# Kernel tuning notes

Hardware: AMD Instinct MI355X
Metric: run time of the kernel (lower is better)

## Reference

```python
import jax, jax.numpy as jnp
import numpy as np

# ---- static problem sizes (full batches: cum[b] = b * max_num) ----
B = 256          # graphs per batch
MAXN, MAXE, MAXC = 128, 256, 64   # max nodes / edges / 2-cells per graph
H = 256          # embed_dim == hidden
L = 4            # num GCNCConv layers
OUT = 10         # out_size
P_N, P_E = 131072, 98304          # up-adjacency pair counts (dim 0, dim 1)
Q_E, Q_C = 131072, 65536          # boundary incidence counts (dim 1, dim 2)


def setup_inputs() -> dict:
    key = jax.random.key(0)
    ks = jax.random.split(key, 24)
    s = 1.0 / np.sqrt(H)
    inp = {}
    # flat cochain features [total_entities, H]
    inp['x_n'] = jax.random.normal(ks[0], (B * MAXN, H), jnp.float32)
    inp['x_e'] = jax.random.normal(ks[1], (B * MAXE, H), jnp.float32)
    inp['x_c'] = jax.random.normal(ks[2], (B * MAXC, H), jnp.float32)
    # node-level up adjacency (pairs of nodes sharing an edge coboundary)
    inp['n_up_b'] = jax.random.randint(ks[3], (P_N,), 0, B, jnp.int32)
    inp['n_up_i'] = jax.random.randint(ks[4], (P_N,), 0, MAXN, jnp.int32)
    inp['n_up_j'] = jax.random.randint(ks[5], (P_N,), 0, MAXN, jnp.int32)
    inp['n_up_e'] = jax.random.randint(ks[6], (P_N,), 0, MAXE, jnp.int32)
    # edge-level up adjacency (pairs of edges sharing a cell coboundary)
    inp['e_up_b'] = jax.random.randint(ks[7], (P_E,), 0, B, jnp.int32)
    inp['e_up_i'] = jax.random.randint(ks[8], (P_E,), 0, MAXE, jnp.int32)
    inp['e_up_j'] = jax.random.randint(ks[9], (P_E,), 0, MAXE, jnp.int32)
    inp['e_up_c'] = jax.random.randint(ks[10], (P_E,), 0, MAXC, jnp.int32)
    # boundary incidence: edges -> nodes, cells -> edges
    inp['eb_b'] = jax.random.randint(ks[11], (Q_E,), 0, B, jnp.int32)
    inp['eb_i'] = jax.random.randint(ks[12], (Q_E,), 0, MAXE, jnp.int32)
    inp['eb_j'] = jax.random.randint(ks[13], (Q_E,), 0, MAXN, jnp.int32)
    inp['cb_b'] = jax.random.randint(ks[14], (Q_C,), 0, B, jnp.int32)
    inp['cb_i'] = jax.random.randint(ks[15], (Q_C,), 0, MAXC, jnp.int32)
    inp['cb_j'] = jax.random.randint(ks[16], (Q_C,), 0, MAXE, jnp.int32)
    # learned parameters
    inp['Wself'] = jax.random.normal(ks[17], (L, 3, H, H), jnp.float32) * s
    inp['bself'] = jnp.zeros((L, 3, H), jnp.float32)
    inp['Wupx'] = jax.random.normal(ks[18], (L, 2, H, H), jnp.float32) * s
    inp['Wupa'] = jax.random.normal(ks[19], (L, 2, H, H), jnp.float32) * s
    inp['Wb'] = jax.random.normal(ks[20], (L, 2, H, H), jnp.float32) * s
    inp['Wp'] = jax.random.normal(ks[21], (H, H), jnp.float32) * s
    inp['Wp_ref'] = jax.random.normal(ks[22], (H, H), jnp.float32) * s
    inp['bp'] = jnp.zeros((H,), jnp.float32)
    k2 = jax.random.split(ks[23], 4)
    inp['W1'] = jax.random.normal(k2[0], (3, H, 2 * H), jnp.float32) * s
    inp['b1'] = jnp.zeros((3, 2 * H), jnp.float32)
    inp['W2'] = jax.random.normal(k2[1], (2 * H, OUT), jnp.float32) * s
    inp['b2'] = jnp.zeros((OUT,), jnp.float32)
    return inp


def reference(x_n, x_e, x_c, n_up_b, n_up_i, n_up_j, n_up_e,
              e_up_b, e_up_i, e_up_j, e_up_c, eb_b, eb_i, eb_j,
              cb_b, cb_i, cb_j, Wself, bself, Wupx, Wupa, Wb,
              Wp, Wp_ref, bp, W1, b1, W2, b2):
    relu = jax.nn.relu
    # dense per-batch boundary adjacencies (scatter-set, as in init_data_to_dense_gcnc)
    b_adj_e = jnp.zeros((B, MAXE, MAXN), jnp.float32).at[eb_b, eb_i, eb_j].set(1.0)
    b_adj_c = jnp.zeros((B, MAXC, MAXE), jnp.float32).at[cb_b, cb_i, cb_j].set(1.0)
    # flat gather/scatter indices: cum[b] = b * max_num (full batches)
    n_i = n_up_b * MAXN + n_up_i
    n_j = n_up_b * MAXN + n_up_j
    n_a = n_up_b * MAXE + n_up_e   # up_attr_idx into edge features
    e_i = e_up_b * MAXE + e_up_i
    e_j = e_up_b * MAXE + e_up_j
    e_a = e_up_b * MAXC + e_up_c   # up_attr_idx into cell features
    xs = [x_n, x_e, x_c]
    refs = xs  # init features used by pool_weight
    for l in range(L):
        xn, xe, xc = xs
        # up messages: msg = relu(W x_j + W' up_attr), scatter-sum to receiver
        up_n = jax.ops.segment_sum(
            relu(xn[n_j] @ Wupx[l, 0] + xe[n_a] @ Wupa[l, 0]),
            n_i, num_segments=B * MAXN)
        up_e = jax.ops.segment_sum(
            relu(xe[e_j] @ Wupx[l, 1] + xc[e_a] @ Wupa[l, 1]),
            e_i, num_segments=B * MAXE)
        # boundary messages: dense masked matmul with incidence matrices
        bd_e = jnp.einsum('ben,bnh->beh', b_adj_e,
                          xn.reshape(B, MAXN, H)).reshape(B * MAXE, H) @ Wb[l, 0]
        bd_c = jnp.einsum('bce,beh->bch', b_adj_c,
                          xe.reshape(B, MAXE, H)).reshape(B * MAXC, H) @ Wb[l, 1]
        xs = [relu(xn @ Wself[l, 0] + bself[l, 0] + up_n),
              relu(xe @ Wself[l, 1] + bself[l, 1] + up_e + bd_e),
              relu(xc @ Wself[l, 2] + bself[l, 2] + bd_c)]
    # pool weights (gating vs. init features) + sum readout per dimension
    maxs = (MAXN, MAXE, MAXC)
    pooled = []
    for i in range(3):
        w = jax.nn.sigmoid(xs[i] @ Wp + refs[i] @ Wp_ref + bp)
        pooled.append((w * xs[i]).reshape(B, maxs[i], H).sum(axis=1))  # [B,H]
    h = sum(relu(pooled[i] @ W1[i] + b1[i]) for i in range(3))  # final_readout='sum'
    return h @ W2 + b2  # [B, OUT]
```

## Files before the change

kernel.cpp:

```cpp
#include <hip/hip_runtime.h>
#include <cstdint>
#include <cstddef>

typedef unsigned short u16;
typedef __bf16 bf16x8 __attribute__((ext_vector_type(8)));
typedef float f32x4 __attribute__((ext_vector_type(4)));
typedef unsigned short u16x8 __attribute__((ext_vector_type(8)));

#define NB   256
#define MAXN 128
#define MAXE 256
#define MAXC 64
#define HD   256
#define NLAYER 4
#define PN 131072
#define PE 98304
#define QE 131072
#define QC 65536
#define MN (NB*MAXN)
#define ME (NB*MAXE)
#define MC (NB*MAXC)

#define SEG_N  0
#define SEG_E  (MN)
#define SEG_EB (MN + ME)
#define SEG_CB (MN + 2*ME)
#define HTOT   (MN + 2*ME + MC)
#define UPTOT  (PN + PE)

__device__ __forceinline__ float bf2f(u16 u){
  union{unsigned int i; float f;} x; x.i = ((unsigned int)u) << 16; return x.f;
}
__device__ __forceinline__ u16 f2bf(float f){
  union{float f; unsigned int i;} x; x.f = f;
  unsigned int r = x.i + 0x7fffu + ((x.i >> 16) & 1u);
  return (u16)(r >> 16);
}
__device__ __forceinline__ f32x4 MFMA(bf16x8 a, bf16x8 b, f32x4 c){
  return __builtin_amdgcn_mfma_f32_16x16x32_bf16(a, b, c, 0, 0, 0);
}
__device__ __forceinline__ void gl_lds16(const u16* g, u16* l){
  __builtin_amdgcn_global_load_lds(
      (const __attribute__((address_space(1))) unsigned int*)g,
      (__attribute__((address_space(3))) unsigned int*)l, 16, 0, 0);
}

__global__ void detect_dtype(const u16* __restrict__ x, int* __restrict__ flag){
  if(threadIdx.x == 0 && blockIdx.x == 0){
    int cnt = 0;
    for(int i = 0; i < 64; i++){
      int e = (x[i] >> 7) & 0xFF;
      if(e >= 118 && e <= 136) cnt++;
    }
    *flag = (cnt >= 50) ? 1 : 0;
  }
}

__global__ __launch_bounds__(256) void conv_bf(const void* __restrict__ src, u16* __restrict__ dst,
                                               long n, const int* __restrict__ flag){
  long i = ((long)blockIdx.x * 256 + threadIdx.x) * 8;
  if(i >= n) return;
  const int isbf = *flag;
  if(i + 8 <= n){
    if(isbf){
      *reinterpret_cast<u16x8*>(dst + i) = *reinterpret_cast<const u16x8*>((const u16*)src + i);
    }else{
      const float* s = (const float*)src + i;
      float4 a = *reinterpret_cast<const float4*>(s);
      float4 b = *reinterpret_cast<const float4*>(s + 4);
      u16x8 o;
      o[0]=f2bf(a.x); o[1]=f2bf(a.y); o[2]=f2bf(a.z); o[3]=f2bf(a.w);
      o[4]=f2bf(b.x); o[5]=f2bf(b.y); o[6]=f2bf(b.z); o[7]=f2bf(b.w);
      *reinterpret_cast<u16x8*>(dst + i) = o;
    }
  }else{
    for(long e = i; e < n; e++)
      dst[e] = isbf ? ((const u16*)src)[e] : f2bf(((const float*)src)[e]);
  }
}

__global__ __launch_bounds__(256) void conv_f2b(const float* __restrict__ s, u16* __restrict__ d, long n){
  long i = ((long)blockIdx.x * 256 + threadIdx.x) * 8;
  if(i >= n) return;
  float4 a = *reinterpret_cast<const float4*>(s + i);
  float4 b = *reinterpret_cast<const float4*>(s + i + 4);
  u16x8 o;
  o[0]=f2bf(a.x); o[1]=f2bf(a.y); o[2]=f2bf(a.z); o[3]=f2bf(a.w);
  o[4]=f2bf(b.x); o[5]=f2bf(b.y); o[6]=f2bf(b.z); o[7]=f2bf(b.w);
  *reinterpret_cast<u16x8*>(d + i) = o;
}

__global__ __launch_bounds__(256) void zero_f4(float* __restrict__ p, long n4){
  long i = (long)blockIdx.x * blockDim.x + threadIdx.x;
  if(i >= n4) return;
  float4 z = {0.f, 0.f, 0.f, 0.f};
  *reinterpret_cast<float4*>(p + i * 4) = z;
}

__global__ void wt_transpose(const void* __restrict__ src, u16* __restrict__ dst,
                             const int* __restrict__ flag){
  __shared__ u16 t[16][17];
  int m = blockIdx.z;
  int n0 = blockIdx.x * 16, k0 = blockIdx.y * 16;
  size_t sidx = (size_t)m * 65536 + (size_t)(k0 + threadIdx.y) * 256 + n0 + threadIdx.x;
  u16 v = (*flag) ? ((const u16*)src)[sidx] : f2bf(((const float*)src)[sidx]);
  t[threadIdx.y][threadIdx.x] = v;
  __syncthreads();
  dst[(size_t)m * 65536 + (size_t)(n0 + threadIdx.y) * 256 + (k0 + threadIdx.x)] =
      t[threadIdx.x][threadIdx.y];
}

__global__ void w1_transpose(const u16* __restrict__ src, u16* __restrict__ dst){
  __shared__ u16 t[16][17];
  int i = blockIdx.z;
  int o0 = blockIdx.x * 16, k0 = blockIdx.y * 16;
  t[threadIdx.y][threadIdx.x] =
      src[(size_t)i * 131072 + (size_t)(k0 + threadIdx.y) * 512 + o0 + threadIdx.x];
  __syncthreads();
  dst[(size_t)i * 131072 + (size_t)(o0 + threadIdx.y) * 256 + (k0 + threadIdx.x)] =
      t[threadIdx.x][threadIdx.y];
}

__global__ void dedup_kernel(const int* __restrict__ bb, const int* __restrict__ bi,
                             const int* __restrict__ bj, unsigned int* __restrict__ mask,
                             unsigned char* __restrict__ valid, int Q, int maxI, int maxJ){
  int q = blockIdx.x * blockDim.x + threadIdx.x;
  if(q >= Q) return;
  int s = (bb[q] * maxI + bi[q]) * maxJ + bj[q];
  unsigned int bit = 1u << (s & 31);
  unsigned int old = atomicOr(&mask[s >> 5], bit);
  valid[q] = (old & bit) ? 0 : 1;
}

__global__ __launch_bounds__(256) void hist_up(const int* __restrict__ pb, const int* __restrict__ pi,
                                               int maxI, int segBase, int* __restrict__ hist, int P){
  int p = blockIdx.x * 256 + threadIdx.x;
  if(p >= P) return;
  atomicAdd(&hist[segBase + pb[p] * maxI + pi[p]], 1);
}
__global__ __launch_bounds__(256) void hist_bd(const int* __restrict__ bb, const int* __restrict__ bi,
                                               const unsigned char* __restrict__ valid,
                                               int maxI, int segBase, int* __restrict__ hist, int Q){
  int q = blockIdx.x * 256 + threadIdx.x;
  if(q >= Q || !valid[q]) return;
  atomicAdd(&hist[segBase + bb[q] * maxI + bi[q]], 1);
}

__global__ __launch_bounds__(256) void scan1(const int* __restrict__ hist, int* __restrict__ bsum){
  __shared__ int s[256];
  int t = threadIdx.x;
  long base = (long)blockIdx.x * 1024 + t * 4;
  int4 v = *reinterpret_cast<const int4*>(hist + base);
  s[t] = v.x + v.y + v.z + v.w;
  __syncthreads();
  for(int st = 128; st > 0; st >>= 1){
    if(t < st) s[t] += s[t + st];
    __syncthreads();
  }
  if(t == 0) bsum[blockIdx.x] = s[0];
}
__global__ __launch_bounds__(256) void scan2(int* __restrict__ bsum, int nb){
  __shared__ int s[256];
  int t = threadIdx.x;
  int v = (t < nb) ? bsum[t] : 0;
  s[t] = v;
  __syncthreads();
  for(int st = 1; st < 256; st <<= 1){
    int u = (t >= st) ? s[t - st] : 0;
    __syncthreads();
    s[t] += u;
    __syncthreads();
  }
  if(t < nb) bsum[t] = s[t] - v;
}
__global__ __launch_bounds__(256) void scan3(const int* __restrict__ hist, const int* __restrict__ bsum,
                                             int* __restrict__ off, int* __restrict__ cur){
  __shared__ int s[256];
  int t = threadIdx.x;
  long base = (long)blockIdx.x * 1024 + t * 4;
  int4 v = *reinterpret_cast<const int4*>(hist + base);
  int sum = v.x + v.y + v.z + v.w;
  s[t] = sum;
  __syncthreads();
  for(int st = 1; st < 256; st <<= 1){
    int u = (t >= st) ? s[t - st] : 0;
    __syncthreads();
    s[t] += u;
    __syncthreads();
  }
  int excl = s[t] - sum + bsum[blockIdx.x];
  int4 o;
  o.x = excl; o.y = o.x + v.x; o.z = o.y + v.y; o.w = o.z + v.z;
  *reinterpret_cast<int4*>(off + base) = o;
  *reinterpret_cast<int4*>(cur + base) = o;
}

__global__ __launch_bounds__(256) void fill_up(const int* __restrict__ pb, const int* __restrict__ pi,
    const int* __restrict__ pj, const int* __restrict__ pa, int maxI, int maxA, int segBase,
    int* __restrict__ cur, int2* __restrict__ csrUp, int P){
  int p = blockIdx.x * 256 + threadIdx.x;
  if(p >= P) return;
  int b = pb[p];
  int pos = atomicAdd(&cur[segBase + b * maxI + pi[p]], 1);
  int2 e; e.x = b * maxI + pj[p]; e.y = b * maxA + pa[p];
  csrUp[pos] = e;
}
__global__ __launch_bounds__(256) void fill_bd(const int* __restrict__ bb, const int* __restrict__ bi,
    const int* __restrict__ bj, const unsigned char* __restrict__ valid, int maxI, int maxJ,
    int segBase, int* __restrict__ cur, int* __restrict__ csrBd, int Q){
  int q = blockIdx.x * 256 + threadIdx.x;
  if(q >= Q || !valid[q]) return;
  int b = bb[q];
  int pos = atomicAdd(&cur[segBase + b * maxI + bi[q]], 1);
  csrBd[pos - UPTOT] = b * maxJ + bj[q];
}

template<int HAS_UP, int HAS_BD>
__global__ __launch_bounds__(256) void gather_k(
    const u16* __restrict__ Y, const u16* __restrict__ Z, const u16* __restrict__ BD,
    const int2* __restrict__ csrUp, const int* __restrict__ csrBd,
    const int* __restrict__ off, const int* __restrict__ deg,
    int upBase, int bdBase, u16* __restrict__ ACC, int rowLo){
  const int nb = gridDim.x;
  int bx = blockIdx.x;
  if((nb & 7) == 0) bx = (bx & 7) * (nb >> 3) + (bx >> 3);
  const int row = rowLo + bx * 4 + (threadIdx.x >> 6);
  const int lane = threadIdx.x & 63;
  const int c = lane * 4;
  float a0 = 0.f, a1 = 0.f, a2 = 0.f, a3 = 0.f;
  if(HAS_UP){
    int s = off[upBase + row];
    int d = deg[upBase + row];
    for(int k = 0; k < d; k++){
      int2 e = csrUp[s + k];
      const ushort4 y = *reinterpret_cast<const ushort4*>(Y + (size_t)e.x * 256 + c);
      const ushort4 z = *reinterpret_cast<const ushort4*>(Z + (size_t)e.y * 256 + c);
      a0 += fmaxf(bf2f(y.x) + bf2f(z.x), 0.f);
      a1 += fmaxf(bf2f(y.y) + bf2f(z.y), 0.f);
      a2 += fmaxf(bf2f(y.z) + bf2f(z.z), 0.f);
      a3 += fmaxf(bf2f(y.w) + bf2f(z.w), 0.f);
    }
  }
  if(HAS_BD){
    int s = off[bdBase + row] - UPTOT;
    int d = deg[bdBase + row];
    for(int k = 0; k < d; k++){
      int j = csrBd[s + k];
      const ushort4 x = *reinterpret_cast<const ushort4*>(BD + (size_t)j * 256 + c);
      a0 += bf2f(x.x); a1 += bf2f(x.y); a2 += bf2f(x.z); a3 += bf2f(x.w);
    }
  }
  ushort4 o; o.x = f2bf(a0); o.y = f2bf(a1); o.z = f2bf(a2); o.w = f2bf(a3);
  *reinterpret_cast<ushort4*>(ACC + (size_t)(row - rowLo) * 256 + c) = o;
}

template<int MODE>
__global__ __launch_bounds__(256) void gemm_b(const u16* A, const u16* __restrict__ WT,
                                              u16* C, const u16* __restrict__ ACC,
                                              const u16* __restrict__ bias,
                                              const u16* A2, const u16* __restrict__ WT2){
  __shared__ u16 lA[2][64 * 64];
  __shared__ u16 lB[2][256 * 64];
  const int t = threadIdx.x;
  const int lane = t & 63, wv = t >> 6;
  const int wn = wv;
  const int r = lane & 15, q = lane >> 4;
  const int rsw = r & 7;
  const size_t m0 = (size_t)blockIdx.x * 64;
  const int lrow = lane >> 3, lchk = lane & 7;
  const int csw = lchk ^ lrow;

  f32x4 acc[4][4];
#pragma unroll
  for(int i = 0; i < 4; i++)
#pragma unroll
    for(int j = 0; j < 4; j++) acc[i][j] = {0.f, 0.f, 0.f, 0.f};

  const int NT = (MODE == 3) ? 8 : 4;

  auto stage = [&](int tt, int buf){
    const u16* Ap = (MODE == 3 && tt >= 4) ? A2 : A;
    const u16* Wp = (MODE == 3 && tt >= 4) ? WT2 : WT;
    const int k0 = (tt & 3) * 64;
#pragma unroll
    for(int i = 0; i < 2; i++){
      const int row = wv * 16 + i * 8 + lrow;
      gl_lds16(Ap + (m0 + row) * 256 + k0 + csw * 8, &lA[buf][(wv * 16 + i * 8) * 64]);
    }
#pragma unroll
    for(int j = 0; j < 8; j++){
      const int n = wv * 64 + j * 8 + lrow;
      gl_lds16(Wp + (size_t)n * 256 + k0 + csw * 8, &lB[buf][(wv * 64 + j * 8) * 64]);
    }
  };

  stage(0, 0);
  stage(1, 1);

#pragma unroll
  for(int tt = 0; tt < NT; tt++){
    const int cur = tt & 1;
    if(tt < NT - 1) asm volatile("s_waitcnt vmcnt(10)" ::: "memory");
    else            asm volatile("s_waitcnt vmcnt(0)" ::: "memory");
    __builtin_amdgcn_s_barrier();
    __builtin_amdgcn_s_setprio(1);
#pragma unroll
    for(int ks = 0; ks < 2; ks++){
      bf16x8 af[4], bfr[4];
#pragma unroll
      for(int i = 0; i < 4; i++)
        af[i] = *reinterpret_cast<const bf16x8*>(
            &lA[cur][(i * 16 + r) * 64 + (((ks * 4 + q) ^ rsw) * 8)]);
#pragma unroll
      for(int j = 0; j < 4; j++)
        bfr[j] = *reinterpret_cast<const bf16x8*>(
            &lB[cur][(wn * 64 + j * 16 + r) * 64 + (((ks * 4 + q) ^ rsw) * 8)]);
#pragma unroll
      for(int i = 0; i < 4; i++)
#pragma unroll
        for(int j = 0; j < 4; j++) acc[i][j] = MFMA(bfr[j], af[i], acc[i][j]);
    }
    __builtin_amdgcn_s_setprio(0);
    __builtin_amdgcn_s_barrier();
    if(tt + 2 < NT) stage(tt + 2, cur);
  }

#pragma unroll
  for(int i = 0; i < 4; i++){
    const size_t row = m0 + i * 16 + r;
#pragma unroll
    for(int j = 0; j < 4; j++){
      const int col = wn * 64 + j * 16 + q * 4;
      const size_t idx = row * 256 + col;
      f32x4 v = acc[i][j];
      ushort4 o;
      if(MODE == 2){
        const ushort4 a4 = *reinterpret_cast<const ushort4*>(ACC + idx);
        const ushort4 b4 = *reinterpret_cast<const ushort4*>(bias + col);
        o.x = f2bf(fmaxf(v[0] + bf2f(a4.x) + bf2f(b4.x), 0.f));
        o.y = f2bf(fmaxf(v[1] + bf2f(a4.y) + bf2f(b4.y), 0.f));
        o.z = f2bf(fmaxf(v[2] + bf2f(a4.z) + bf2f(b4.z), 0.f));
        o.w = f2bf(fmaxf(v[3] + bf2f(a4.w) + bf2f(b4.w), 0.f));
      }else{
        o.x = f2bf(v[0]); o.y = f2bf(v[1]); o.z = f2bf(v[2]); o.w = f2bf(v[3]);
      }
      *reinterpret_cast<ushort4*>(C + idx) = o;
    }
  }
}

__global__ __launch_bounds__(256) void pool_reduce(const u16* __restrict__ G, const u16* __restrict__ bpv,
    const u16* __restrict__ X, float* __restrict__ pooled, int maxR, int rowsPerBlk){
  int b = blockIdx.x, h = threadIdx.x;
  int r0 = blockIdx.y * rowsPerBlk;
  float bias = bf2f(bpv[h]);
  float acc = 0.f;
  for(int r = r0; r < r0 + rowsPerBlk; r++){
    size_t o = ((size_t)b * maxR + r) * 256 + h;
    float t = bf2f(G[o]) + bias;
    float w = 1.f / (1.f + __expf(-t));
    acc += w * bf2f(X[o]);
  }
  atomicAdd(&pooled[b * 256 + h], acc);
}

__global__ __launch_bounds__(512) void readout1_mfma(const u16* __restrict__ Ab,
                                                     const u16* __restrict__ W1t,
                                                     const u16* __restrict__ b1,
                                                     float* __restrict__ hbuf){
  __shared__ u16 lA[2][128 * 64];
  __shared__ u16 lB[2][256 * 64];
  const int t = threadIdx.x;
  const int lane = t & 63, wv = t >> 6;
  const int wm = wv >> 2, wn = wv & 3;
  const int r = lane & 15, q = lane >> 4;
  const int rsw = r & 7;
  const int b0 = blockIdx.x * 128;
  const int o0 = blockIdx.y * 256;
  const int lrow = lane >> 3, lchk = lane & 7;
  const int csw = lchk ^ lrow;

  f32x4 acc[4][4], facc[4][4];
#pragma unroll
  for(int i = 0; i < 4; i++)
#pragma unroll
    for(int j = 0; j < 4; j++){ acc[i][j] = {0.f,0.f,0.f,0.f}; facc[i][j] = {0.f,0.f,0.f,0.f}; }

  auto stage = [&](int tt, int buf){
    const int ii = tt >> 2, k0 = (tt & 3) * 64;
    const u16* Ap = Ab + (size_t)ii * 65536;
    const u16* Wp = W1t + (size_t)ii * 131072;
#pragma unroll
    for(int i = 0; i < 2; i++){
      const int row = i * 64 + wv * 8 + lrow;
      gl_lds16(Ap + (size_t)(b0 + row) * 256 + k0 + csw * 8, &lA[buf][(i * 64 + wv * 8) * 64]);
    }
#pragma unroll
    for(int j = 0; j < 4; j++){
      const int n = j * 64 + wv * 8 + lrow;
      gl_lds16(Wp + (size_t)(o0 + n) * 256 + k0 + csw * 8, &lB[buf][(j * 64 + wv * 8) * 64]);
    }
  };

  stage(0, 0);
  stage(1, 1);

#pragma unroll
  for(int tt = 0; tt < 12; tt++){
    const int cur = tt & 1;
    if(tt < 11) asm volatile("s_waitcnt vmcnt(6)" ::: "memory");
    else        asm volatile("s_waitcnt vmcnt(0)" ::: "memory");
    __builtin_amdgcn_s_barrier();
#pragma unroll
    for(int ks = 0; ks < 2; ks++){
      bf16x8 af[4], bfr[4];
#pragma unroll
      for(int i = 0; i < 4; i++)
        af[i] = *reinterpret_cast<const bf16x8*>(
            &lA[cur][(wm * 64 + i * 16 + r) * 64 + (((ks * 4 + q) ^ rsw) * 8)]);
#pragma unroll
      for(int j = 0; j < 4; j++)
        bfr[j] = *reinterpret_cast<const bf16x8*>(
            &lB[cur][(wn * 64 + j * 16 + r) * 64 + (((ks * 4 + q) ^ rsw) * 8)]);
#pragma unroll
      for(int i = 0; i < 4; i++)
#pragma unroll
        for(int j = 0; j < 4; j++) acc[i][j] = MFMA(bfr[j], af[i], acc[i][j]);
    }
    if((tt & 3) == 3){
      const int ib = tt >> 2;
#pragma unroll
      for(int i = 0; i < 4; i++)
#pragma unroll
        for(int j = 0; j < 4; j++){
          const int col = o0 + wn * 64 + j * 16 + q * 4;
          const ushort4 b4 = *reinterpret_cast<const ushort4*>(b1 + ib * 512 + col);
          facc[i][j][0] += fmaxf(acc[i][j][0] + bf2f(b4.x), 0.f);
          facc[i][j][1] += fmaxf(acc[i][j][1] + bf2f(b4.y), 0.f);
          facc[i][j][2] += fmaxf(acc[i][j][2] + bf2f(b4.z), 0.f);
          facc[i][j][3] += fmaxf(acc[i][j][3] + bf2f(b4.w), 0.f);
          acc[i][j] = {0.f, 0.f, 0.f, 0.f};
        }
    }
    __builtin_amdgcn_s_barrier();
    if(tt + 2 < 12) stage(tt + 2, cur);
  }

#pragma unroll
  for(int i = 0; i < 4; i++){
    const int row = b0 + wm * 64 + i * 16 + r;
#pragma unroll
    for(int j = 0; j < 4; j++){
      const int col = o0 + wn * 64 + j * 16 + q * 4;
      *reinterpret_cast<f32x4*>(hbuf + (size_t)row * 512 + col) = facc[i][j];
    }
  }
}

__global__ __launch_bounds__(64) void readout2(const float* __restrict__ hbuf, const u16* __restrict__ W2,
                                               const u16* __restrict__ b2, void* __restrict__ out,
                                               const int* __restrict__ flag){
  int b = blockIdx.x, o = threadIdx.x;
  if(o >= 10) return;
  float a = bf2f(b2[o]);
  for(int k = 0; k < 512; k++) a += hbuf[(size_t)b * 512 + k] * bf2f(W2[k * 10 + o]);
  if(*flag) ((u16*)out)[b * 10 + o] = f2bf(a);
  else      ((float*)out)[b * 10 + o] = a;
}

extern "C" void kernel_launch(void* const* d_in, const int* in_sizes, int n_in,
                              void* d_out, int out_size, void* d_ws, size_t ws_size,
                              hipStream_t stream){
  const void* x_n = d_in[0];
  const void* x_e = d_in[1];
  const void* x_c = d_in[2];
  const int* n_up_b = (const int*)d_in[3];
  const int* n_up_i = (const int*)d_in[4];
  const int* n_up_j = (const int*)d_in[5];
  const int* n_up_e = (const int*)d_in[6];
  const int* e_up_b = (const int*)d_in[7];
  const int* e_up_i = (const int*)d_in[8];
  const int* e_up_j = (const int*)d_in[9];
  const int* e_up_c = (const int*)d_in[10];
  const int* eb_b = (const int*)d_in[11];
  const int* eb_i = (const int*)d_in[12];
  const int* eb_j = (const int*)d_in[13];
  const int* cb_b = (const int*)d_in[14];
  const int* cb_i = (const int*)d_in[15];
  const int* cb_j = (const int*)d_in[16];

  char* base = (char*)d_ws; size_t off0 = 0;
  auto alloc = [&](size_t n)->char*{ char* p = base + off0; off0 = (off0 + n + 255) & ~(size_t)255; return p; };
  u16* xn = (u16*)alloc((size_t)MN * HD * 2);
  u16* xe = (u16*)alloc((size_t)ME * HD * 2);
  u16* xc = (u16*)alloc((size_t)MC * HD * 2);
  u16* BIG1 = (u16*)alloc((size_t)ME * HD * 2);
  u16* SMa  = (u16*)alloc((size_t)MN * HD * 2);
  u16* SMb  = (u16*)alloc((size_t)MN * HD * 2);
  u16* ACC  = (u16*)alloc((size_t)16384 * HD * 4);
  u16* wt = (u16*)alloc((size_t)38 * 65536 * 2);
  unsigned int* mask_e = (unsigned int*)alloc((size_t)NB * MAXE * MAXN / 8);
  unsigned int* mask_c = (unsigned int*)alloc((size_t)NB * MAXC * MAXE / 8);
  unsigned char* valid_e = (unsigned char*)alloc(QE);
  unsigned char* valid_c = (unsigned char*)alloc(QC);
  float* pooled = (float*)alloc((size_t)3 * NB * HD * 4);
  float* hbuf   = (float*)alloc((size_t)NB * 512 * 4);
  int* flag     = (int*)alloc(256);
  int2* csrUp   = (int2*)alloc((size_t)UPTOT * 8);
  int* csrBd    = (int*)alloc((size_t)(QE + QC) * 4);
  int* hist     = (int*)alloc((size_t)HTOT * 4);
  int* offA     = (int*)alloc((size_t)HTOT * 4);
  int* bsum     = (int*)alloc(1024);
  u16* W1t      = (u16*)alloc((size_t)3 * 512 * 256 * 2);
  u16* pooledb  = (u16*)alloc((size_t)3 * NB * HD * 2);
  int* cur      = (int*)pooled;

  u16* wtSelf = wt;
  u16* wtUpx  = wt + (size_t)12 * 65536;
  u16* wtUpa  = wt + (size_t)20 * 65536;
  u16* wtB    = wt + (size_t)28 * 65536;
  u16* wtP    = wt + (size_t)36 * 65536;
  u16* wtPref = wt + (size_t)37 * 65536;

  u16* W1c = (u16*)mask_e;
  u16* b1c = W1c + 393216;
  u16* W2c = b1c + 1536;
  u16* b2c = W2c + 5120;
  u16* bsc = b2c + 16;
  u16* bpc = bsc + 3072;

  auto convN = [&](const void* s, u16* d, long n){
    long blk = (n + 8*256 - 1) / (8*256);
    conv_bf<<<(int)blk, 256, 0, stream>>>(s, d, n, flag);
  };

  detect_dtype<<<1, 64, 0, stream>>>((const u16*)x_n, flag);
  zero_f4<<<(65536 + 255)/256, 256, 0, stream>>>((float*)mask_e, 65536);
  zero_f4<<<(32768 + 255)/256, 256, 0, stream>>>((float*)mask_c, 32768);
  dedup_kernel<<<QE/256, 256, 0, stream>>>(eb_b, eb_i, eb_j, mask_e, valid_e, QE, MAXE, MAXN);
  dedup_kernel<<<QC/256, 256, 0, stream>>>(cb_b, cb_i, cb_j, mask_c, valid_c, QC, MAXC, MAXE);

  wt_transpose<<<dim3(16,16,12), dim3(16,16), 0, stream>>>(d_in[17], wtSelf, flag);
  wt_transpose<<<dim3(16,16,8),  dim3(16,16), 0, stream>>>(d_in[19], wtUpx,  flag);
  wt_transpose<<<dim3(16,16,8),  dim3(16,16), 0, stream>>>(d_in[20], wtUpa,  flag);
  wt_transpose<<<dim3(16,16,8),  dim3(16,16), 0, stream>>>(d_in[21], wtB,    flag);
  wt_transpose<<<dim3(16,16,1),  dim3(16,16), 0, stream>>>(d_in[22], wtP,    flag);
  wt_transpose<<<dim3(16,16,1),  dim3(16,16), 0, stream>>>(d_in[23], wtPref, flag);
  convN(x_n, xn, (long)MN * HD);
  convN(x_e, xe, (long)ME * HD);
  convN(x_c, xc, (long)MC * HD);
  convN(d_in[18], bsc, 3072);
  convN(d_in[24], bpc, 256);
  convN(d_in[25], W1c, 393216);
  convN(d_in[26], b1c, 1536);
  convN(d_in[27], W2c, 5120);
  convN(d_in[28], b2c, 10);
  w1_transpose<<<dim3(32,16,3), dim3(16,16), 0, stream>>>(W1c, W1t);

  zero_f4<<<(HTOT/4 + 255)/256, 256, 0, stream>>>((float*)hist, HTOT/4);
  hist_up<<<PN/256, 256, 0, stream>>>(n_up_b, n_up_i, MAXN, SEG_N,  hist, PN);
  hist_up<<<PE/256, 256, 0, stream>>>(e_up_b, e_up_i, MAXE, SEG_E,  hist, PE);
  hist_bd<<<QE/256, 256, 0, stream>>>(eb_b, eb_i, valid_e, MAXE, SEG_EB, hist, QE);
  hist_bd<<<QC/256, 256, 0, stream>>>(cb_b, cb_i, valid_c, MAXC, SEG_CB, hist, QC);
  scan1<<<HTOT/1024, 256, 0, stream>>>(hist, bsum);
  scan2<<<1, 256, 0, stream>>>(bsum, HTOT/1024);
  scan3<<<HTOT/1024, 256, 0, stream>>>(hist, bsum, offA, cur);
  fill_up<<<PN/256, 256, 0, stream>>>(n_up_b, n_up_i, n_up_j, n_up_e, MAXN, MAXE, SEG_N, cur, csrUp, PN);
  fill_up<<<PE/256, 256, 0, stream>>>(e_up_b, e_up_i, e_up_j, e_up_c, MAXE, MAXC, SEG_E, cur, csrUp, PE);
  fill_bd<<<QE/256, 256, 0, stream>>>(eb_b, eb_i, eb_j, valid_e, MAXE, MAXN, SEG_EB, cur, csrBd, QE);
  fill_bd<<<QC/256, 256, 0, stream>>>(cb_b, cb_i, cb_j, valid_c, MAXC, MAXE, SEG_CB, cur, csrBd, QC);

  for(int l = 0; l < NLAYER; l++){
    const u16* Wupx0 = wtUpx + (size_t)(l*2+0) * 65536;
    const u16* Wupx1 = wtUpx + (size_t)(l*2+1) * 65536;
    const u16* Wupa0 = wtUpa + (size_t)(l*2+0) * 65536;
    const u16* Wupa1 = wtUpa + (size_t)(l*2+1) * 65536;
    const u16* Wb0   = wtB   + (size_t)(l*2+0) * 65536;
    const u16* Wb1   = wtB   + (size_t)(l*2+1) * 65536;
    const u16* Ws0   = wtSelf + (size_t)(l*3+0) * 65536;
    const u16* Ws1   = wtSelf + (size_t)(l*3+1) * 65536;
    const u16* Ws2   = wtSelf + (size_t)(l*3+2) * 65536;
    const u16* bs0 = bsc + (size_t)(l*3+0) * HD;
    const u16* bs1 = bsc + (size_t)(l*3+1) * HD;
    const u16* bs2 = bsc + (size_t)(l*3+2) * HD;

    gemm_b<0><<<MN/64, 256, 0, stream>>>(xn, Wupx0, SMa, nullptr, nullptr, nullptr, nullptr);
    gemm_b<0><<<ME/64, 256, 0, stream>>>(xe, Wupa0, BIG1, nullptr, nullptr, nullptr, nullptr);
    gemm_b<0><<<MN/64, 256, 0, stream>>>(xn, Wb0, SMb, nullptr, nullptr, nullptr, nullptr);
    for(int h = 0; h < 2; h++){
      int lo = h * (MN/2);
      gather_k<1,0><<<(MN/2)/4, 256, 0, stream>>>(SMa, BIG1, nullptr, csrUp, csrBd,
                                                  offA, hist, SEG_N, 0, ACC, lo);
      gemm_b<2><<<(MN/2)/64, 256, 0, stream>>>(xn + (size_t)lo * HD, Ws0,
                                               xn + (size_t)lo * HD, ACC, bs0, nullptr, nullptr);
    }

    gemm_b<0><<<MC/64, 256, 0, stream>>>(xc, Wupa1, SMa, nullptr, nullptr, nullptr, nullptr);
    gemm_b<0><<<ME/64, 256, 0, stream>>>(xe, Wb1, BIG1, nullptr, nullptr, nullptr, nullptr);
    gather_k<0,1><<<MC/4, 256, 0, stream>>>(nullptr, nullptr, BIG1, csrUp, csrBd,
                                            offA, hist, 0, SEG_CB, ACC, 0);
    gemm_b<2><<<MC/64, 256, 0, stream>>>(xc, Ws2, xc, ACC, bs2, nullptr, nullptr);

    gemm_b<0><<<ME/64, 256, 0, stream>>>(xe, Wupx1, BIG1, nullptr, nullptr, nullptr, nullptr);
    for(int h = 0; h < 2; h++){
      int lo = h * (ME/2);
      gather_k<1,1><<<(ME/2)/4, 256, 0, stream>>>(BIG1, SMa, SMb, csrUp, csrBd,
                                                  offA, hist, SEG_E, SEG_EB, ACC, lo);
      gemm_b<2><<<(ME/2)/64, 256, 0, stream>>>(xe + (size_t)lo * HD, Ws1,
                                               xe + (size_t)lo * HD, ACC, bs1, nullptr, nullptr);
    }
  }

  u16* REF = SMa;
  {
    long np4 = (long)3 * NB * HD / 4;
    zero_f4<<<(int)((np4 + 255)/256), 256, 0, stream>>>(pooled, np4);
  }
  convN(x_n, REF, (long)MN * HD);
  gemm_b<3><<<MN/64, 256, 0, stream>>>(xn, wtP, BIG1, nullptr, nullptr, REF, wtPref);
  pool_reduce<<<dim3(NB,2), 256, 0, stream>>>(BIG1, bpc, xn, pooled, MAXN, MAXN/2);

  convN(x_e, REF, (long)ME * HD);
  gemm_b<3><<<ME/64, 256, 0, stream>>>(xe, wtP, BIG1, nullptr, nullptr, REF, wtPref);
  pool_reduce<<<dim3(NB,4), 256, 0, stream>>>(BIG1, bpc, xe, pooled + (size_t)NB*HD, MAXE, MAXE/4);

  convN(x_c, REF, (long)MC * HD);
  gemm_b<3><<<MC/64, 256, 0, stream>>>(xc, wtP, BIG1, nullptr, nullptr, REF, wtPref);
  pool_reduce<<<dim3(NB,1), 256, 0, stream>>>(BIG1, bpc, xc, pooled + (size_t)2*NB*HD, MAXC, MAXC);

  conv_f2b<<<96, 256, 0, stream>>>(pooled, pooledb, (long)3 * NB * HD);
  readout1_mfma<<<dim3(2,2), 512, 0, stream>>>(pooledb, W1t, b1c, hbuf);
  readout2<<<NB, 64, 0, stream>>>(hbuf, W2c, b2c, d_out, flag);
}
```

Measured before the change: 1.464 ms.

## Batch independent kernels into multi-segment launches and drop half-splits

```diff
diff --git a/kernel.cpp b/kernel.cpp
--- a/kernel.cpp
+++ b/kernel.cpp
@@ -56,27 +56,52 @@
   }
 }
 
-__global__ __launch_bounds__(256) void conv_bf(const void* __restrict__ src, u16* __restrict__ dst,
-                                               long n, const int* __restrict__ flag){
-  long i = ((long)blockIdx.x * 256 + threadIdx.x) * 8;
-  if(i >= n) return;
-  const int isbf = *flag;
+__device__ __forceinline__ void convSpan(const void* s, u16* d, long n, long i, int isbf){
   if(i + 8 <= n){
     if(isbf){
-      *reinterpret_cast<u16x8*>(dst + i) = *reinterpret_cast<const u16x8*>((const u16*)src + i);
+      *reinterpret_cast<u16x8*>(d + i) = *reinterpret_cast<const u16x8*>((const u16*)s + i);
     }else{
-      const float* s = (const float*)src + i;
-      float4 a = *reinterpret_cast<const float4*>(s);
-      float4 b = *reinterpret_cast<const float4*>(s + 4);
+      const float* sp = (const float*)s + i;
+      float4 a = *reinterpret_cast<const float4*>(sp);
+      float4 b = *reinterpret_cast<const float4*>(sp + 4);
       u16x8 o;
       o[0]=f2bf(a.x); o[1]=f2bf(a.y); o[2]=f2bf(a.z); o[3]=f2bf(a.w);
       o[4]=f2bf(b.x); o[5]=f2bf(b.y); o[6]=f2bf(b.z); o[7]=f2bf(b.w);
-      *reinterpret_cast<u16x8*>(dst + i) = o;
+      *reinterpret_cast<u16x8*>(d + i) = o;
     }
   }else{
     for(long e = i; e < n; e++)
-      dst[e] = isbf ? ((const u16*)src)[e] : f2bf(((const float*)src)[e]);
-  }
+      d[e] = isbf ? ((const u16*)s)[e] : f2bf(((const float*)s)[e]);
+  }
+}
+
+__global__ __launch_bounds__(256) void conv3(const void* __restrict__ s0, u16* __restrict__ d0,
+                                             const void* __restrict__ s1, u16* __restrict__ d1,
+                                             const void* __restrict__ s2, u16* __restrict__ d2,
+                                             const int* __restrict__ flag){
+  const long U0 = (long)MN * HD / 8, U1 = (long)ME * HD / 8, U2 = (long)MC * HD / 8;
+  long u = (long)blockIdx.x * 256 + threadIdx.x;
+  const int isbf = *flag;
+  if(u < U0){ convSpan(s0, d0, (long)MN * HD, u * 8, isbf); return; }
+  u -= U0;
+  if(u < U1){ convSpan(s1, d1, (long)ME * HD, u * 8, isbf); return; }
+  u -= U1;
+  if(u < U2) convSpan(s2, d2, (long)MC * HD, u * 8, isbf);
+}
+
+__global__ __launch_bounds__(256) void conv_params(
+    const void* sW1, u16* dW1, const void* sb1, u16* db1,
+    const void* sW2, u16* dW2, const void* sb2, u16* db2,
+    const void* sbs, u16* dbs, const void* sbp, u16* dbp,
+    const int* __restrict__ flag){
+  long u = (long)blockIdx.x * 256 + threadIdx.x;
+  const int isbf = *flag;
+  if(u < 49152){ convSpan(sW1, dW1, 393216, u * 8, isbf); return; } u -= 49152;
+  if(u < 192)  { convSpan(sb1, db1, 1536,   u * 8, isbf); return; } u -= 192;
+  if(u < 640)  { convSpan(sW2, dW2, 5120,   u * 8, isbf); return; } u -= 640;
+  if(u < 2)    { convSpan(sb2, db2, 10,     u * 8, isbf); return; } u -= 2;
+  if(u < 384)  { convSpan(sbs, dbs, 3072,   u * 8, isbf); return; } u -= 384;
+  if(u < 32)     convSpan(sbp, dbp, 256,    u * 8, isbf);
 }
 
 __global__ __launch_bounds__(256) void conv_f2b(const float* __restrict__ s, u16* __restrict__ d, long n){
@@ -97,10 +122,19 @@
   *reinterpret_cast<float4*>(p + i * 4) = z;
 }
 
-__global__ void wt_transpose(const void* __restrict__ src, u16* __restrict__ dst,
-                             const int* __restrict__ flag){
+__global__ void wt_all(const void* __restrict__ pSelf, const void* __restrict__ pUpx,
+                       const void* __restrict__ pUpa, const void* __restrict__ pB,
+                       const void* __restrict__ pP, const void* __restrict__ pPref,
+                       u16* __restrict__ wt, const int* __restrict__ flag){
   __shared__ u16 t[16][17];
-  int m = blockIdx.z;
+  int z = blockIdx.z;
+  const void* src; int m; u16* dst;
+  if(z < 12)      { src = pSelf; m = z;      dst = wt; }
+  else if(z < 20) { src = pUpx;  m = z - 12; dst = wt + (size_t)12 * 65536; }
+  else if(z < 28) { src = pUpa;  m = z - 20; dst = wt + (size_t)20 * 65536; }
+  else if(z < 36) { src = pB;    m = z - 28; dst = wt + (size_t)28 * 65536; }
+  else if(z == 36){ src = pP;    m = 0;      dst = wt + (size_t)36 * 65536; }
+  else            { src = pPref; m = 0;      dst = wt + (size_t)37 * 65536; }
   int n0 = blockIdx.x * 16, k0 = blockIdx.y * 16;
   size_t sidx = (size_t)m * 65536 + (size_t)(k0 + threadIdx.y) * 256 + n0 + threadIdx.x;
   u16 v = (*flag) ? ((const u16*)src)[sidx] : f2bf(((const float*)src)[sidx]);
@@ -132,18 +166,26 @@
   valid[q] = (old & bit) ? 0 : 1;
 }
 
-__global__ __launch_bounds__(256) void hist_up(const int* __restrict__ pb, const int* __restrict__ pi,
-                                               int maxI, int segBase, int* __restrict__ hist, int P){
-  int p = blockIdx.x * 256 + threadIdx.x;
-  if(p >= P) return;
-  atomicAdd(&hist[segBase + pb[p] * maxI + pi[p]], 1);
-}
-__global__ __launch_bounds__(256) void hist_bd(const int* __restrict__ bb, const int* __restrict__ bi,
-                                               const unsigned char* __restrict__ valid,
-                                               int maxI, int segBase, int* __restrict__ hist, int Q){
-  int q = blockIdx.x * 256 + threadIdx.x;
-  if(q >= Q || !valid[q]) return;
-  atomicAdd(&hist[segBase + bb[q] * maxI + bi[q]], 1);
+__global__ __launch_bounds__(256) void hist_all(
+    const int* __restrict__ nub, const int* __restrict__ nui,
+    const int* __restrict__ eub, const int* __restrict__ eui,
+    const int* __restrict__ ebb, const int* __restrict__ ebi, const unsigned char* __restrict__ ve,
+    const int* __restrict__ cbb, const int* __restrict__ cbi, const unsigned char* __restrict__ vc,
+    int* __restrict__ hist){
+  int bx = blockIdx.x, t = threadIdx.x;
+  if(bx < PN/256){
+    int p = bx * 256 + t;
+    atomicAdd(&hist[SEG_N + nub[p] * MAXN + nui[p]], 1);
+  }else if(bx < PN/256 + PE/256){
+    int p = (bx - PN/256) * 256 + t;
+    atomicAdd(&hist[SEG_E + eub[p] * MAXE + eui[p]], 1);
+  }else if(bx < PN/256 + PE/256 + QE/256){
+    int q = (bx - PN/256 - PE/256) * 256 + t;
+    if(ve[q]) atomicAdd(&hist[SEG_EB + ebb[q] * MAXE + ebi[q]], 1);
+  }else{
+    int q = (bx - PN/256 - PE/256 - QE/256) * 256 + t;
+    if(vc[q]) atomicAdd(&hist[SEG_CB + cbb[q] * MAXC + cbi[q]], 1);
+  }
 }
 
 __global__ __launch_bounds__(256) void scan1(const int* __restrict__ hist, int* __restrict__ bsum){
@@ -195,24 +237,40 @@
   *reinterpret_cast<int4*>(cur + base) = o;
 }
 
-__global__ __launch_bounds__(256) void fill_up(const int* __restrict__ pb, const int* __restrict__ pi,
-    const int* __restrict__ pj, const int* __restrict__ pa, int maxI, int maxA, int segBase,
-    int* __restrict__ cur, int2* __restrict__ csrUp, int P){
-  int p = blockIdx.x * 256 + threadIdx.x;
-  if(p >= P) return;
-  int b = pb[p];
-  int pos = atomicAdd(&cur[segBase + b * maxI + pi[p]], 1);
-  int2 e; e.x = b * maxI + pj[p]; e.y = b * maxA + pa[p];
-  csrUp[pos] = e;
-}
-__global__ __launch_bounds__(256) void fill_bd(const int* __restrict__ bb, const int* __restrict__ bi,
-    const int* __restrict__ bj, const unsigned char* __restrict__ valid, int maxI, int maxJ,
-    int segBase, int* __restrict__ cur, int* __restrict__ csrBd, int Q){
-  int q = blockIdx.x * 256 + threadIdx.x;
-  if(q >= Q || !valid[q]) return;
-  int b = bb[q];
-  int pos = atomicAdd(&cur[segBase + b * maxI + bi[q]], 1);
-  csrBd[pos - UPTOT] = b * maxJ + bj[q];
+__global__ __launch_bounds__(256) void fill_all(
+    const int* __restrict__ nub, const int* __restrict__ nui,
+    const int* __restrict__ nuj, const int* __restrict__ nue,
+    const int* __restrict__ eub, const int* __restrict__ eui,
+    const int* __restrict__ euj, const int* __restrict__ euc,
+    const int* __restrict__ ebb, const int* __restrict__ ebi,
+    const int* __restrict__ ebj, const unsigned char* __restrict__ ve,
+    const int* __restrict__ cbb, const int* __restrict__ cbi,
+    const int* __restrict__ cbj, const unsigned char* __restrict__ vc,
+    int* __restrict__ cur, int2* __restrict__ csrUp, int* __restrict__ csrBd){
+  int bx = blockIdx.x, t = threadIdx.x;
+  if(bx < PN/256){
+    int p = bx * 256 + t; int b = nub[p];
+    int pos = atomicAdd(&cur[SEG_N + b * MAXN + nui[p]], 1);
+    int2 e; e.x = b * MAXN + nuj[p]; e.y = b * MAXE + nue[p];
+    csrUp[pos] = e;
+  }else if(bx < PN/256 + PE/256){
+    int p = (bx - PN/256) * 256 + t; int b = eub[p];
+    int pos = atomicAdd(&cur[SEG_E + b * MAXE + eui[p]], 1);
+    int2 e; e.x = b * MAXE + euj[p]; e.y = b * MAXC + euc[p];
+    csrUp[pos] = e;
+  }else if(bx < PN/256 + PE/256 + QE/256){
+    int q = (bx - PN/256 - PE/256) * 256 + t;
+    if(!ve[q]) return;
+    int b = ebb[q];
+    int pos = atomicAdd(&cur[SEG_EB + b * MAXE + ebi[q]], 1);
+    csrBd[pos - UPTOT] = b * MAXN + ebj[q];
+  }else{
+    int q = (bx - PN/256 - PE/256 - QE/256) * 256 + t;
+    if(!vc[q]) return;
+    int b = cbb[q];
+    int pos = atomicAdd(&cur[SEG_CB + b * MAXC + cbi[q]], 1);
+    csrBd[pos - UPTOT] = b * MAXE + cbj[q];
+  }
 }
 
 template<int HAS_UP, int HAS_BD>
@@ -255,18 +313,24 @@
 }
 
 template<int MODE>
-__global__ __launch_bounds__(256) void gemm_b(const u16* A, const u16* __restrict__ WT,
-                                              u16* C, const u16* __restrict__ ACC,
-                                              const u16* __restrict__ bias,
-                                              const u16* A2, const u16* __restrict__ WT2){
+__global__ __launch_bounds__(256) void gemm_k(
+    const u16* P0, const u16* Q0, u16* C0, int n0,
+    const u16* P1, const u16* Q1, u16* C1, int n1,
+    const u16* P2, const u16* Q2, u16* C2,
+    const u16* __restrict__ S1, const u16* __restrict__ S2,
+    const u16* __restrict__ ACC, const u16* __restrict__ bias){
   __shared__ u16 lA[2][64 * 64];
   __shared__ u16 lB[2][256 * 64];
+  int bx = blockIdx.x;
+  const u16* P = P0; const u16* Q = Q0; u16* C = C0;
+  if(bx >= n0 + n1){ bx -= n0 + n1; P = P2; Q = Q2; C = C2; }
+  else if(bx >= n0){ bx -= n0;      P = P1; Q = Q1; C = C1; }
   const int t = threadIdx.x;
   const int lane = t & 63, wv = t >> 6;
   const int wn = wv;
   const int r = lane & 15, q = lane >> 4;
   const int rsw = r & 7;
-  const size_t m0 = (size_t)blockIdx.x * 64;
+  const size_t m0 = (size_t)bx * 64;
   const int lrow = lane >> 3, lchk = lane & 7;
   const int csw = lchk ^ lrow;
 
@@ -279,8 +343,8 @@
   const int NT = (MODE == 3) ? 8 : 4;
 
   auto stage = [&](int tt, int buf){
-    const u16* Ap = (MODE == 3 && tt >= 4) ? A2 : A;
-    const u16* Wp = (MODE == 3 && tt >= 4) ? WT2 : WT;
+    const u16* Ap = (MODE == 3) ? ((tt >= 4) ? Q : P) : P;
+    const u16* Wp = (MODE == 3) ? ((tt >= 4) ? S2 : S1) : Q;
     const int k0 = (tt & 3) * 64;
 #pragma unroll
     for(int i = 0; i < 2; i++){
@@ -349,19 +413,25 @@
   }
 }
 
-__global__ __launch_bounds__(256) void pool_reduce(const u16* __restrict__ G, const u16* __restrict__ bpv,
-    const u16* __restrict__ X, float* __restrict__ pooled, int maxR, int rowsPerBlk){
-  int b = blockIdx.x, h = threadIdx.x;
-  int r0 = blockIdx.y * rowsPerBlk;
+__global__ __launch_bounds__(256) void pool_all(
+    const u16* __restrict__ Gn, const u16* __restrict__ Ge, const u16* __restrict__ Gc,
+    const u16* __restrict__ bpv,
+    const u16* __restrict__ Xn, const u16* __restrict__ Xe, const u16* __restrict__ Xc,
+    float* __restrict__ pooled){
+  int b = blockIdx.x, h = threadIdx.x, y = blockIdx.y;
+  const u16 *G, *X; float* out; int maxR, r0;
+  if(y < 2)      { G = Gn; X = Xn; out = pooled;                    maxR = MAXN; r0 = y * 64; }
+  else if(y < 6) { G = Ge; X = Xe; out = pooled + (size_t)NB * HD;  maxR = MAXE; r0 = (y - 2) * 64; }
+  else           { G = Gc; X = Xc; out = pooled + (size_t)2*NB*HD;  maxR = MAXC; r0 = 0; }
   float bias = bf2f(bpv[h]);
   float acc = 0.f;
-  for(int r = r0; r < r0 + rowsPerBlk; r++){
+  for(int r = r0; r < r0 + 64; r++){
     size_t o = ((size_t)b * maxR + r) * 256 + h;
     float t = bf2f(G[o]) + bias;
     float w = 1.f / (1.f + __expf(-t));
     acc += w * bf2f(X[o]);
   }
-  atomicAdd(&pooled[b * 256 + h], acc);
+  atomicAdd(&out[b * 256 + h], acc);
 }
 
 __global__ __launch_bounds__(512) void readout1_mfma(const u16* __restrict__ Ab,
@@ -497,7 +567,7 @@
   u16* BIG1 = (u16*)alloc((size_t)ME * HD * 2);
   u16* SMa  = (u16*)alloc((size_t)MN * HD * 2);
   u16* SMb  = (u16*)alloc((size_t)MN * HD * 2);
-  u16* ACC  = (u16*)alloc((size_t)16384 * HD * 4);
+  u16* ACC  = (u16*)alloc((size_t)ME * HD * 2);
   u16* wt = (u16*)alloc((size_t)38 * 65536 * 2);
   unsigned int* mask_e = (unsigned int*)alloc((size_t)NB * MAXE * MAXN / 8);
   unsigned int* mask_c = (unsigned int*)alloc((size_t)NB * MAXC * MAXE / 8);
@@ -529,46 +599,27 @@
   u16* bsc = b2c + 16;
   u16* bpc = bsc + 3072;
 
-  auto convN = [&](const void* s, u16* d, long n){
-    long blk = (n + 8*256 - 1) / (8*256);
-    conv_bf<<<(int)blk, 256, 0, stream>>>(s, d, n, flag);
-  };
-
   detect_dtype<<<1, 64, 0, stream>>>((const u16*)x_n, flag);
-  zero_f4<<<(65536 + 255)/256, 256, 0, stream>>>((float*)mask_e, 65536);
-  zero_f4<<<(32768 + 255)/256, 256, 0, stream>>>((float*)mask_c, 32768);
+  zero_f4<<<(98304 + 255)/256, 256, 0, stream>>>((float*)mask_e, 98304);
   dedup_kernel<<<QE/256, 256, 0, stream>>>(eb_b, eb_i, eb_j, mask_e, valid_e, QE, MAXE, MAXN);
   dedup_kernel<<<QC/256, 256, 0, stream>>>(cb_b, cb_i, cb_j, mask_c, valid_c, QC, MAXC, MAXE);
 
-  wt_transpose<<<dim3(16,16,12), dim3(16,16), 0, stream>>>(d_in[17], wtSelf, flag);
-  wt_transpose<<<dim3(16,16,8),  dim3(16,16), 0, stream>>>(d_in[19], wtUpx,  flag);
-  wt_transpose<<<dim3(16,16,8),  dim3(16,16), 0, stream>>>(d_in[20], wtUpa,  flag);
-  wt_transpose<<<dim3(16,16,8),  dim3(16,16), 0, stream>>>(d_in[21], wtB,    flag);
-  wt_transpose<<<dim3(16,16,1),  dim3(16,16), 0, stream>>>(d_in[22], wtP,    flag);
-  wt_transpose<<<dim3(16,16,1),  dim3(16,16), 0, stream>>>(d_in[23], wtPref, flag);
-  convN(x_n, xn, (long)MN * HD);
-  convN(x_e, xe, (long)ME * HD);
-  convN(x_c, xc, (long)MC * HD);
-  convN(d_in[18], bsc, 3072);
-  convN(d_in[24], bpc, 256);
-  convN(d_in[25], W1c, 393216);
-  convN(d_in[26], b1c, 1536);
-  convN(d_in[27], W2c, 5120);
-  convN(d_in[28], b2c, 10);
+  wt_all<<<dim3(16,16,38), dim3(16,16), 0, stream>>>(d_in[17], d_in[19], d_in[20],
+                                                     d_in[21], d_in[22], d_in[23], wt, flag);
+  conv3<<<14336, 256, 0, stream>>>(x_n, xn, x_e, xe, x_c, xc, flag);
+  conv_params<<<197, 256, 0, stream>>>(d_in[25], W1c, d_in[26], b1c, d_in[27], W2c,
+                                       d_in[28], b2c, d_in[18], bsc, d_in[24], bpc, flag);
   w1_transpose<<<dim3(32,16,3), dim3(16,16), 0, stream>>>(W1c, W1t);
 
   zero_f4<<<(HTOT/4 + 255)/256, 256, 0, stream>>>((float*)hist, HTOT/4);
-  hist_up<<<PN/256, 256, 0, stream>>>(n_up_b, n_up_i, MAXN, SEG_N,  hist, PN);
-  hist_up<<<PE/256, 256, 0, stream>>>(e_up_b, e_up_i, MAXE, SEG_E,  hist, PE);
-  hist_bd<<<QE/256, 256, 0, stream>>>(eb_b, eb_i, valid_e, MAXE, SEG_EB, hist, QE);
-  hist_bd<<<QC/256, 256, 0, stream>>>(cb_b, cb_i, valid_c, MAXC, SEG_CB, hist, QC);
+  hist_all<<<PN/256 + PE/256 + QE/256 + QC/256, 256, 0, stream>>>(
+      n_up_b, n_up_i, e_up_b, e_up_i, eb_b, eb_i, valid_e, cb_b, cb_i, valid_c, hist);
   scan1<<<HTOT/1024, 256, 0, stream>>>(hist, bsum);
   scan2<<<1, 256, 0, stream>>>(bsum, HTOT/1024);
   scan3<<<HTOT/1024, 256, 0, stream>>>(hist, bsum, offA, cur);
-  fill_up<<<PN/256, 256, 0, stream>>>(n_up_b, n_up_i, n_up_j, n_up_e, MAXN, MAXE, SEG_N, cur, csrUp, PN);
-  fill_up<<<PE/256, 256, 0, stream>>>(e_up_b, e_up_i, e_up_j, e_up_c, MAXE, MAXC, SEG_E, cur, csrUp, PE);
-  fill_bd<<<QE/256, 256, 0, stream>>>(eb_b, eb_i, eb_j, valid_e, MAXE, MAXN, SEG_EB, cur, csrBd, QE);
-  fill_bd<<<QC/256, 256, 0, stream>>>(cb_b, cb_i, cb_j, valid_c, MAXC, MAXE, SEG_CB, cur, csrBd, QC);
+  fill_all<<<PN/256 + PE/256 + QE/256 + QC/256, 256, 0, stream>>>(
+      n_up_b, n_up_i, n_up_j, n_up_e, e_up_b, e_up_i, e_up_j, e_up_c,
+      eb_b, eb_i, eb_j, valid_e, cb_b, cb_i, cb_j, valid_c, cur, csrUp, csrBd);
 
   for(int l = 0; l < NLAYER; l++){
     const u16* Wupx0 = wtUpx + (size_t)(l*2+0) * 65536;
@@ -584,49 +635,40 @@
     const u16* bs1 = bsc + (size_t)(l*3+1) * HD;
     const u16* bs2 = bsc + (size_t)(l*3+2) * HD;
 
-    gemm_b<0><<<MN/64, 256, 0, stream>>>(xn, Wupx0, SMa, nullptr, nullptr, nullptr, nullptr);
-    gemm_b<0><<<ME/64, 256, 0, stream>>>(xe, Wupa0, BIG1, nullptr, nullptr, nullptr, nullptr);
-    gemm_b<0><<<MN/64, 256, 0, stream>>>(xn, Wb0, SMb, nullptr, nullptr, nullptr, nullptr);
-    for(int h = 0; h < 2; h++){
-      int lo = h * (MN/2);
-      gather_k<1,0><<<(MN/2)/4, 256, 0, stream>>>(SMa, BIG1, nullptr, csrUp, csrBd,
-                                                  offA, hist, SEG_N, 0, ACC, lo);
-      gemm_b<2><<<(MN/2)/64, 256, 0, stream>>>(xn + (size_t)lo * HD, Ws0,
-                                               xn + (size_t)lo * HD, ACC, bs0, nullptr, nullptr);
-    }
-
-    gemm_b<0><<<MC/64, 256, 0, stream>>>(xc, Wupa1, SMa, nullptr, nullptr, nullptr, nullptr);
-    gemm_b<0><<<ME/64, 256, 0, stream>>>(xe, Wb1, BIG1, nullptr, nullptr, nullptr, nullptr);
+    gemm_k<0><<<MN/64 + ME/64 + MN/64, 256, 0, stream>>>(
+        xn, Wupx0, SMa, MN/64, xe, Wupa0, BIG1, ME/64, xn, Wb0, SMb,
+        nullptr, nullptr, nullptr, nullptr);
+    gather_k<1,0><<<MN/4, 256, 0, stream>>>(SMa, BIG1, nullptr, csrUp, csrBd,
+                                            offA, hist, SEG_N, 0, ACC, 0);
+    gemm_k<2><<<MN/64, 256, 0, stream>>>(xn, Ws0, xn, MN/64, xn, Ws0, xn, 0, xn, Ws0, xn,
+                                         nullptr, nullptr, ACC, bs0);
+
+    gemm_k<0><<<MC/64 + ME/64, 256, 0, stream>>>(
+        xc, Wupa1, SMa, MC/64, xe, Wb1, BIG1, ME/64, xc, Wupa1, SMa,
+        nullptr, nullptr, nullptr, nullptr);
     gather_k<0,1><<<MC/4, 256, 0, stream>>>(nullptr, nullptr, BIG1, csrUp, csrBd,
                                             offA, hist, 0, SEG_CB, ACC, 0);
-    gemm_b<2><<<MC/64, 256, 0, stream>>>(xc, Ws2, xc, ACC, bs2, nullptr, nullptr);
-
-    gemm_b<0><<<ME/64, 256, 0, stream>>>(xe, Wupx1, BIG1, nullptr, nullptr, nullptr, nullptr);
-    for(int h = 0; h < 2; h++){
-      int lo = h * (ME/2);
-      gather_k<1,1><<<(ME/2)/4, 256, 0, stream>>>(BIG1, SMa, SMb, csrUp, csrBd,
-                                                  offA, hist, SEG_E, SEG_EB, ACC, lo);
-      gemm_b<2><<<(ME/2)/64, 256, 0, stream>>>(xe + (size_t)lo * HD, Ws1,
-                                               xe + (size_t)lo * HD, ACC, bs1, nullptr, nullptr);
-    }
-  }
-
-  u16* REF = SMa;
+    gemm_k<2><<<MC/64, 256, 0, stream>>>(xc, Ws2, xc, MC/64, xc, Ws2, xc, 0, xc, Ws2, xc,
+                                         nullptr, nullptr, ACC, bs2);
+
+    gemm_k<0><<<ME/64, 256, 0, stream>>>(
+        xe, Wupx1, BIG1, ME/64, xe, Wupx1, BIG1, 0, xe, Wupx1, BIG1,
+        nullptr, nullptr, nullptr, nullptr);
+    gather_k<1,1><<<ME/4, 256, 0, stream>>>(BIG1, SMa, SMb, csrUp, csrBd,
+                                            offA, hist, SEG_E, SEG_EB, ACC, 0);
+    gemm_k<2><<<ME/64, 256, 0, stream>>>(xe, Ws1, xe, ME/64, xe, Ws1, xe, 0, xe, Ws1, xe,
+                                         nullptr, nullptr, ACC, bs1);
+  }
+
+  conv3<<<14336, 256, 0, stream>>>(x_n, SMa, x_e, ACC, x_c, SMb, flag);
   {
     long np4 = (long)3 * NB * HD / 4;
     zero_f4<<<(int)((np4 + 255)/256), 256, 0, stream>>>(pooled, np4);
   }
-  convN(x_n, REF, (long)MN * HD);
-  gemm_b<3><<<MN/64, 256, 0, stream>>>(xn, wtP, BIG1, nullptr, nullptr, REF, wtPref);
-  pool_reduce<<<dim3(NB,2), 256, 0, stream>>>(BIG1, bpc, xn, pooled, MAXN, MAXN/2);
-
-  convN(x_e, REF, (long)ME * HD);
-  gemm_b<3><<<ME/64, 256, 0, stream>>>(xe, wtP, BIG1, nullptr, nullptr, REF, wtPref);
-  pool_reduce<<<dim3(NB,4), 256, 0, stream>>>(BIG1, bpc, xe, pooled + (size_t)NB*HD, MAXE, MAXE/4);
-
-  convN(x_c, REF, (long)MC * HD);
-  gemm_b<3><<<MC/64, 256, 0, stream>>>(xc, wtP, BIG1, nullptr, nullptr, REF, wtPref);
-  pool_reduce<<<dim3(NB,1), 256, 0, stream>>>(BIG1, bpc, xc, pooled + (size_t)2*NB*HD, MAXC, MAXC);
+  gemm_k<3><<<MN/64 + ME/64 + MC/64, 256, 0, stream>>>(
+      xn, SMa, SMa, MN/64, xe, ACC, ACC, ME/64, xc, SMb, SMb,
+      wtP, wtPref, nullptr, nullptr);
+  pool_all<<<dim3(NB, 7), 256, 0, stream>>>(SMa, ACC, SMb, bpc, xn, xe, xc, pooled);
 
   conv_f2b<<<96, 256, 0, stream>>>(pooled, pooledb, (long)3 * NB * HD);
   readout1_mfma<<<dim3(2,2), 512, 0, stream>>>(pooledb, W1t, b1c, hbuf);
```

After: 1.291 ms. 11.8% less time.
